# Kernel tuning notes

Measured on AMD Instinct MI355X. Metric: run time of the kernel, lower is better.

## Reference

```python
import jax, jax.numpy as jnp
import numpy as np

N_NODES = 50000
N_EDGES = 800000  # includes N_NODES self-loops so every node has in-degree >= 1
D_IN = 64
D_OUT = 64


def setup_inputs() -> dict:
    key = jax.random.key(0)
    k_feat, k_src, k_dst, k_wt, k_wp = jax.random.split(key, 5)
    feat = jax.random.normal(k_feat, (N_NODES, D_IN), dtype=jnp.float32)
    n_rand = N_EDGES - N_NODES
    loops = jnp.arange(N_NODES, dtype=jnp.int64)
    src = jnp.concatenate([loops, jax.random.randint(k_src, (n_rand,), 0, N_NODES, dtype=jnp.int64)])
    dst = jnp.concatenate([loops, jax.random.randint(k_dst, (n_rand,), 0, N_NODES, dtype=jnp.int64)])
    scale = 1.0 / np.sqrt(D_IN)
    W_theta = jax.random.normal(k_wt, (D_IN, D_OUT), dtype=jnp.float32) * scale
    b_theta = jnp.zeros((D_OUT,), dtype=jnp.float32)
    W_phi = jax.random.normal(k_wp, (D_IN, D_OUT), dtype=jnp.float32) * scale
    b_phi = jnp.zeros((D_OUT,), dtype=jnp.float32)
    return {"feat": feat, "src": src, "dst": dst,
            "W_theta": W_theta, "b_theta": b_theta,
            "W_phi": W_phi, "b_phi": b_phi}


def reference(feat, src, dst, W_theta, b_theta, W_phi, b_phi):
    # Per-edge message: theta(x_dst - x_src)  [fn.v_sub_u then Dense theta]
    diff = feat[dst] - feat[src]                       # [E, D_in]
    theta_e = diff @ W_theta + b_theta                 # [E, D_out]
    # Per-destination-node term: phi(x_dst)  [Dense phi]
    phi = feat @ W_phi + b_phi                         # [N, D_out]
    e = theta_e + phi[dst]                             # [E, D_out]  (fn.e_add_v)
    # Scatter-max aggregation by destination node (fn.max)
    out = jax.ops.segment_max(e, dst, num_segments=feat.shape[0])  # [N, D_out]
    return out
```

## Files before the change

### kernel.cpp

```cpp
#include <hip/hip_runtime.h>
#include <hip/hip_bf16.h>

#define N_NODES 50000
#define N_EDGES 800000
#define D 64
#define NB 391
#define BCAP 4096
#define CHUNK_E 2048
#define NSC 391
#define NSTRIP 3125
#define GEMM_BLKS 196
#define NWAVES 784
#define SPW 4

typedef __attribute__((ext_vector_type(8))) short short8v;
typedef __attribute__((ext_vector_type(4))) float float4v;

__device__ __forceinline__ float b2f(unsigned short h) {
    return __uint_as_float(((unsigned)h) << 16);
}
__device__ __forceinline__ unsigned short f2b(float f) {
    __hip_bfloat16 t = __float2bfloat16(f);
    return *reinterpret_cast<unsigned short*>(&t);
}
__device__ __forceinline__ short f2bs(float f) { return (short)f2b(f); }
__device__ __forceinline__ unsigned f2ord(float f) {
    unsigned u = __float_as_uint(f);
    return (u & 0x80000000u) ? ~u : (u | 0x80000000u);
}
__device__ __forceinline__ float ord2f(unsigned o) {
    return __uint_as_float((o & 0x80000000u) ? (o ^ 0x80000000u) : ~o);
}

__global__ __launch_bounds__(256)
void setup(const void* __restrict__ featv, const void* __restrict__ srcv,
           const void* __restrict__ Wtv, const void* __restrict__ btv,
           const void* __restrict__ Wpv, const void* __restrict__ bpv,
           unsigned* __restrict__ flags, unsigned* __restrict__ c_cur,
           unsigned short* __restrict__ WTfrag, unsigned short* __restrict__ WPfrag,
           float* __restrict__ bias_sum) {
    __shared__ unsigned sf[2];
    const int t = threadIdx.x;
    if (t < 64) {
        const unsigned short* p = (const unsigned short*)featv;
        float x = b2f(p[2 * t]);
        float a = fabsf(x);
        bool insane = !(a <= 64.f) || (x != 0.f && a < 9.3132e-10f);
        unsigned long long m = __ballot(insane);
        if (t == 0) sf[0] = (__popcll(m) >= 8) ? 1u : 0u;
    } else if (t < 128) {
        const int* s32 = (const int*)srcv;
        int v = s32[2 * (t - 64) + 1];
        unsigned long long m = __ballot(v == 0);
        if (t == 64) sf[1] = (__popcll(m) >= 32) ? 1u : 0u;
    }
    __syncthreads();
    const unsigned fp32mode = sf[0];
    if (t < 2) flags[t] = sf[t];
    for (int i = t; i < NB; i += 256) c_cur[i] = 0;
#pragma unroll
    for (int i = 0; i < 16; ++i) {
        int e = i * 256 + t;
        int k = e >> 6, n = e & 63;
        float vt, vp;
        if (fp32mode) {
            vt = ((const float*)Wtv)[e];
            vp = ((const float*)Wpv)[e];
        } else {
            vt = b2f(((const unsigned short*)Wtv)[e]);
            vp = b2f(((const unsigned short*)Wpv)[e]);
        }
        WTfrag[n * 64 + k] = f2b(vt);
        WPfrag[n * 64 + k] = f2b(vp);
    }
    if (t < 64) {
        if (fp32mode)
            bias_sum[t] = ((const float*)btv)[t] + ((const float*)bpv)[t];
        else
            bias_sum[t] = b2f(((const unsigned short*)btv)[t])
                        + b2f(((const unsigned short*)bpv)[t]);
    }
}

__device__ __forceinline__ void loadA_bf16(const short* F, int w, int m, int q,
                                           short8v& A0, short8v& A1) {
    const short* fr = F + (w * 16 + m) * D + q * 8;
    A0 = *(const short8v*)fr;
    A1 = *(const short8v*)(fr + 32);
}
__device__ __forceinline__ void loadA_raw(const float* F, int w, int m, int q,
                                          float4 r[8]) {
    const float* fr = F + (w * 16 + m) * D + q * 8;
    r[0] = *(const float4*)(fr);      r[1] = *(const float4*)(fr + 4);
    r[2] = *(const float4*)(fr + 32); r[3] = *(const float4*)(fr + 36);
}
__device__ __forceinline__ void cvtA(const float4 r[8], short8v& A0, short8v& A1) {
    A0 = (short8v){f2bs(r[0].x), f2bs(r[0].y), f2bs(r[0].z), f2bs(r[0].w),
                   f2bs(r[1].x), f2bs(r[1].y), f2bs(r[1].z), f2bs(r[1].w)};
    A1 = (short8v){f2bs(r[2].x), f2bs(r[2].y), f2bs(r[2].z), f2bs(r[2].w),
                   f2bs(r[3].x), f2bs(r[3].y), f2bs(r[3].z), f2bs(r[3].w)};
}

__global__ __launch_bounds__(256)
void gemm_scatter(const void* __restrict__ featv,
                  const unsigned short* __restrict__ WTfrag,
                  const unsigned short* __restrict__ WPfrag,
                  const float* __restrict__ bias_sum,
                  const void* __restrict__ srcv, const void* __restrict__ dstv,
                  const unsigned* __restrict__ flags,
                  unsigned* __restrict__ c_cur, unsigned* __restrict__ packed,
                  unsigned short* __restrict__ T16, void* __restrict__ outv) {
    const unsigned fp32mode = flags[0];
    if (blockIdx.x < GEMM_BLKS) {
        const int lane = threadIdx.x & 63;
        const int wid  = threadIdx.x >> 6;
        const int wave = blockIdx.x * 4 + wid;
        const int m = lane & 15, q = lane >> 4;

        const short8v* BT = (const short8v*)WTfrag;
        const short8v* BP = (const short8v*)WPfrag;
        short8v Bt0[4], Bt1[4], Bp0[4], Bp1[4];
        float bsv[4];
#pragma unroll
        for (int c = 0; c < 4; ++c) {
            const int col = 16 * c + m;
            Bt0[c] = BT[col * 8 + q];
            Bt1[c] = BT[col * 8 + 4 + q];
            Bp0[c] = BP[col * 8 + q];
            Bp1[c] = BP[col * 8 + 4 + q];
            bsv[c] = bias_sum[col];
        }

        float* Cf  = (float*)outv;
        unsigned short* Ch = (unsigned short*)outv;
        const float* Ff = (const float*)featv;
        const short* Fh = (const short*)featv;

        short8v A0, A1;
        float4 raw[8];
        int w = wave;
        if (fp32mode) { loadA_raw(Ff, min(w, NSTRIP - 1), m, q, raw); cvtA(raw, A0, A1); }
        else          loadA_bf16(Fh, min(w, NSTRIP - 1), m, q, A0, A1);

#pragma unroll
        for (int s = 0; s < SPW; ++s) {
            const int wn = wave + (s + 1) * NWAVES;
            if (s + 1 < SPW) {
                if (fp32mode) loadA_raw(Ff, min(wn, NSTRIP - 1), m, q, raw);
                else          loadA_bf16(Fh, min(wn, NSTRIP - 1), m, q, A0, A1);
            }
            if (w < NSTRIP) {
                short8v Acur0, Acur1;
                if (s + 1 < SPW && !fp32mode) {
                    loadA_bf16(Fh, w, m, q, Acur0, Acur1);
                } else if (!fp32mode) {
                    Acur0 = A0; Acur1 = A1;
                } else {
                    Acur0 = A0; Acur1 = A1;
                }
#pragma unroll
                for (int c = 0; c < 4; ++c) {
                    float4v accT = (float4v){0.f, 0.f, 0.f, 0.f};
                    float4v accP = (float4v){bsv[c], bsv[c], bsv[c], bsv[c]};
                    accT = __builtin_amdgcn_mfma_f32_16x16x32_bf16(Acur0, Bt0[c], accT, 0, 0, 0);
                    accT = __builtin_amdgcn_mfma_f32_16x16x32_bf16(Acur1, Bt1[c], accT, 0, 0, 0);
                    accP = __builtin_amdgcn_mfma_f32_16x16x32_bf16(Acur0, Bp0[c], accP, 0, 0, 0);
                    accP = __builtin_amdgcn_mfma_f32_16x16x32_bf16(Acur1, Bp1[c], accP, 0, 0, 0);
                    const int col = 16 * c + m;
#pragma unroll
                    for (int r = 0; r < 4; ++r) {
                        const int row = w * 16 + q * 4 + r;
                        T16[row * D + col] = f2b(accT[r]);
                        if (fp32mode) Cf[row * D + col] = accT[r] + accP[r];
                        else          Ch[row * D + col] = f2b(accT[r] + accP[r]);
                    }
                }
            }
            w = wn;
            if (fp32mode && s + 1 < SPW) cvtA(raw, A0, A1);
        }
    } else {
        __shared__ unsigned h[NB];
        const int t = threadIdx.x;
        for (int i = t; i < NB; i += 256) h[i] = 0;
        __syncthreads();
        const unsigned idx64 = flags[1];
        const int base = (blockIdx.x - GEMM_BLKS) * CHUNK_E;
        unsigned pk[CHUNK_E / 256];
#pragma unroll
        for (int j = 0; j < CHUNK_E / 256; ++j) {
            int e = base + j * 256 + t;
            unsigned p = 0xFFFFFFFFu;
            if (e < N_EDGES) {
                int s, d;
                if (idx64) {
                    s = (int)((const long long*)srcv)[e];
                    d = (int)((const long long*)dstv)[e];
                } else {
                    s = ((const int*)srcv)[e];
                    d = ((const int*)dstv)[e];
                }
                s = min(max(s, 0), N_NODES - 1);
                d = min(max(d, 0), N_NODES - 1);
                if (s != d) {
                    p = ((unsigned)d << 16) | (unsigned)s;
                    atomicAdd(&h[d >> 7], 1u);
                }
            }
            pk[j] = p;
        }
        __syncthreads();
        for (int i = t; i < NB; i += 256) h[i] = atomicAdd(&c_cur[i], h[i]);
        __syncthreads();
#pragma unroll
        for (int j = 0; j < CHUNK_E / 256; ++j) {
            unsigned p = pk[j];
            if (p != 0xFFFFFFFFu) {
                unsigned bkt = p >> 23;
                unsigned pos = atomicAdd(&h[bkt], 1u);
                if (pos < BCAP)
                    packed[bkt * BCAP + pos] = p;
            }
        }
    }
}

__global__ __launch_bounds__(512)
void bucket_min(const unsigned* __restrict__ c_cur, const unsigned* __restrict__ packed,
                const unsigned short* __restrict__ T16, const unsigned* __restrict__ flags,
                void* __restrict__ outv) {
    __shared__ unsigned mn[128 * 64];
    const unsigned fp32mode = flags[0];
    const int t = threadIdx.x;
    const int b = blockIdx.x;
    const int node0 = b << 7;
    for (int sl = t; sl < 128 * 16; sl += 512) {
        const int row = sl >> 4;
        const int f4 = (sl & 15) << 2;
        unsigned* mp = &mn[row * 64 + f4];
        if (node0 + row < N_NODES) {
            uint2 v = *(const uint2*)(T16 + (node0 + row) * D + f4);
            mp[0] = f2ord(b2f((unsigned short)v.x));
            mp[1] = f2ord(b2f((unsigned short)(v.x >> 16)));
            mp[2] = f2ord(b2f((unsigned short)v.y));
            mp[3] = f2ord(b2f((unsigned short)(v.y >> 16)));
        } else {
            mp[0] = mp[1] = mp[2] = mp[3] = 0xFFFFFFFFu;
        }
    }
    __syncthreads();
    const int cnt = min((int)c_cur[b], BCAP);
    const unsigned* pb = packed + b * BCAP;
    const int lane = t & 63, wv = t >> 6;
    const int g = lane >> 4, fb = (lane & 15) << 2;
    int i = wv * 4 + g;
    for (; i + 96 < cnt; i += 128) {
        unsigned p0 = pb[i],      p1 = pb[i + 32];
        unsigned p2 = pb[i + 64], p3 = pb[i + 96];
        uint2 v0 = *(const uint2*)(T16 + (int)(p0 & 0xFFFFu) * D + fb);
        uint2 v1 = *(const uint2*)(T16 + (int)(p1 & 0xFFFFu) * D + fb);
        uint2 v2 = *(const uint2*)(T16 + (int)(p2 & 0xFFFFu) * D + fb);
        uint2 v3 = *(const uint2*)(T16 + (int)(p3 & 0xFFFFu) * D + fb);
        unsigned* m0p = &mn[(int)((p0 >> 16) & 127u) * 64 + fb];
        unsigned* m1p = &mn[(int)((p1 >> 16) & 127u) * 64 + fb];
        unsigned* m2p = &mn[(int)((p2 >> 16) & 127u) * 64 + fb];
        unsigned* m3p = &mn[(int)((p3 >> 16) & 127u) * 64 + fb];
        atomicMin(m0p + 0, f2ord(b2f((unsigned short)v0.x)));
        atomicMin(m0p + 1, f2ord(b2f((unsigned short)(v0.x >> 16))));
        atomicMin(m0p + 2, f2ord(b2f((unsigned short)v0.y)));
        atomicMin(m0p + 3, f2ord(b2f((unsigned short)(v0.y >> 16))));
        atomicMin(m1p + 0, f2ord(b2f((unsigned short)v1.x)));
        atomicMin(m1p + 1, f2ord(b2f((unsigned short)(v1.x >> 16))));
        atomicMin(m1p + 2, f2ord(b2f((unsigned short)v1.y)));
        atomicMin(m1p + 3, f2ord(b2f((unsigned short)(v1.y >> 16))));
        atomicMin(m2p + 0, f2ord(b2f((unsigned short)v2.x)));
        atomicMin(m2p + 1, f2ord(b2f((unsigned short)(v2.x >> 16))));
        atomicMin(m2p + 2, f2ord(b2f((unsigned short)v2.y)));
        atomicMin(m2p + 3, f2ord(b2f((unsigned short)(v2.y >> 16))));
        atomicMin(m3p + 0, f2ord(b2f((unsigned short)v3.x)));
        atomicMin(m3p + 1, f2ord(b2f((unsigned short)(v3.x >> 16))));
        atomicMin(m3p + 2, f2ord(b2f((unsigned short)v3.y)));
        atomicMin(m3p + 3, f2ord(b2f((unsigned short)(v3.y >> 16))));
    }
    for (; i < cnt; i += 32) {
        unsigned p0 = pb[i];
        uint2 v0 = *(const uint2*)(T16 + (int)(p0 & 0xFFFFu) * D + fb);
        unsigned* m0p = &mn[(int)((p0 >> 16) & 127u) * 64 + fb];
        atomicMin(m0p + 0, f2ord(b2f((unsigned short)v0.x)));
        atomicMin(m0p + 1, f2ord(b2f((unsigned short)(v0.x >> 16))));
        atomicMin(m0p + 2, f2ord(b2f((unsigned short)v0.y)));
        atomicMin(m0p + 3, f2ord(b2f((unsigned short)(v0.y >> 16))));
    }
    __syncthreads();
    for (int sl = t; sl < 128 * 16; sl += 512) {
        const int row = sl >> 4;
        const int node = node0 + row;
        if (node >= N_NODES) break;
        const int f4 = (sl & 15) << 2;
        const unsigned* mp = &mn[row * 64 + f4];
        float m0 = ord2f(mp[0]), m1 = ord2f(mp[1]);
        float m2 = ord2f(mp[2]), m3 = ord2f(mp[3]);
        if (fp32mode) {
            float4* C = (float4*)((float*)outv + node * D + f4);
            float4 c = *C;
            *C = make_float4(c.x - m0, c.y - m1, c.z - m2, c.w - m3);
        } else {
            unsigned short* C = (unsigned short*)outv + node * D + f4;
            uint2 c = *(uint2*)C;
            unsigned lo = (unsigned)f2b(b2f((unsigned short)c.x) - m0)
                        | ((unsigned)f2b(b2f((unsigned short)(c.x >> 16)) - m1) << 16);
            unsigned hi = (unsigned)f2b(b2f((unsigned short)c.y) - m2)
                        | ((unsigned)f2b(b2f((unsigned short)(c.y >> 16)) - m3) << 16);
            *(uint2*)C = make_uint2(lo, hi);
        }
    }
}

extern "C" void kernel_launch(void* const* d_in, const int* in_sizes, int n_in,
                              void* d_out, int out_size, void* d_ws, size_t ws_size,
                              hipStream_t stream) {
    char* p = (char*)d_ws;
    unsigned*       flags    = (unsigned*)p;
    unsigned*       c_cur    = (unsigned*)(p + 256);
    unsigned*       packed   = (unsigned*)(p + 4352);
    unsigned short* T16      = (unsigned short*)(p + 4352 + 6406144);
    unsigned short* WTfrag   = (unsigned short*)(p + 4352 + 6406144 + 6400000);
    unsigned short* WPfrag   = (unsigned short*)(p + 4352 + 6406144 + 6400000 + 8192);
    float*          bias_sum = (float*)(p + 4352 + 6406144 + 6400000 + 16384);

    setup<<<1, 256, 0, stream>>>(d_in[0], d_in[1], d_in[3], d_in[4], d_in[5], d_in[6],
                                 flags, c_cur, WTfrag, WPfrag, bias_sum);
    gemm_scatter<<<GEMM_BLKS + NSC, 256, 0, stream>>>(d_in[0], WTfrag, WPfrag, bias_sum,
                                                      d_in[1], d_in[2], flags,
                                                      c_cur, packed, T16, d_out);
    bucket_min<<<NB, 512, 0, stream>>>(c_cur, packed, T16, flags, d_out);
}
```

Before: 128.9 us.

## Use finer 32-node destination buckets with padded LDS and 16-byte gathers

Destination buckets shrink from 128 nodes to 32 nodes, giving 1563 buckets of capacity 1024 and 256-thread bucket_min blocks, so many more blocks run concurrently. Each lane now gathers 8 bf16 features per edge with a 16-byte load. The shared min table uses a 65-word row stride to cut LDS bank conflicts during atomicMin. The scatter phase also skips the global atomicAdd for empty buckets. The trade-offs are more global bucket counters and a smaller per-bucket capacity that could overflow on skewed degree distributions.

```diff
diff --git a/kernel.cpp b/kernel.cpp
--- a/kernel.cpp
+++ b/kernel.cpp
@@ -4,14 +4,15 @@
 #define N_NODES 50000
 #define N_EDGES 800000
 #define D 64
-#define NB 391
-#define BCAP 4096
+#define NB 1563
+#define BCAP 1024
 #define CHUNK_E 2048
 #define NSC 391
 #define NSTRIP 3125
 #define GEMM_BLKS 196
 #define NWAVES 784
 #define SPW 4
+#define MSTR 65
 
 typedef __attribute__((ext_vector_type(8))) short short8v;
 typedef __attribute__((ext_vector_type(4))) float float4v;
@@ -204,19 +205,22 @@
                 d = min(max(d, 0), N_NODES - 1);
                 if (s != d) {
                     p = ((unsigned)d << 16) | (unsigned)s;
-                    atomicAdd(&h[d >> 7], 1u);
+                    atomicAdd(&h[d >> 5], 1u);
                 }
             }
             pk[j] = p;
         }
         __syncthreads();
-        for (int i = t; i < NB; i += 256) h[i] = atomicAdd(&c_cur[i], h[i]);
+        for (int i = t; i < NB; i += 256) {
+            unsigned c = h[i];
+            h[i] = c ? atomicAdd(&c_cur[i], c) : 0u;
+        }
         __syncthreads();
 #pragma unroll
         for (int j = 0; j < CHUNK_E / 256; ++j) {
             unsigned p = pk[j];
             if (p != 0xFFFFFFFFu) {
-                unsigned bkt = p >> 23;
+                unsigned bkt = p >> 21;
                 unsigned pos = atomicAdd(&h[bkt], 1u);
                 if (pos < BCAP)
                     packed[bkt * BCAP + pos] = p;
@@ -225,19 +229,19 @@
     }
 }
 
-__global__ __launch_bounds__(512)
+__global__ __launch_bounds__(256, 8)
 void bucket_min(const unsigned* __restrict__ c_cur, const unsigned* __restrict__ packed,
                 const unsigned short* __restrict__ T16, const unsigned* __restrict__ flags,
                 void* __restrict__ outv) {
-    __shared__ unsigned mn[128 * 64];
+    __shared__ unsigned mn[32 * MSTR];
     const unsigned fp32mode = flags[0];
     const int t = threadIdx.x;
     const int b = blockIdx.x;
-    const int node0 = b << 7;
-    for (int sl = t; sl < 128 * 16; sl += 512) {
+    const int node0 = b << 5;
+    for (int sl = t; sl < 32 * 16; sl += 256) {
         const int row = sl >> 4;
         const int f4 = (sl & 15) << 2;
-        unsigned* mp = &mn[row * 64 + f4];
+        unsigned* mp = &mn[row * MSTR + f4];
         if (node0 + row < N_NODES) {
             uint2 v = *(const uint2*)(T16 + (node0 + row) * D + f4);
             mp[0] = f2ord(b2f((unsigned short)v.x));
@@ -252,52 +256,53 @@
     const int cnt = min((int)c_cur[b], BCAP);
     const unsigned* pb = packed + b * BCAP;
     const int lane = t & 63, wv = t >> 6;
-    const int g = lane >> 4, fb = (lane & 15) << 2;
-    int i = wv * 4 + g;
-    for (; i + 96 < cnt; i += 128) {
-        unsigned p0 = pb[i],      p1 = pb[i + 32];
-        unsigned p2 = pb[i + 64], p3 = pb[i + 96];
-        uint2 v0 = *(const uint2*)(T16 + (int)(p0 & 0xFFFFu) * D + fb);
-        uint2 v1 = *(const uint2*)(T16 + (int)(p1 & 0xFFFFu) * D + fb);
-        uint2 v2 = *(const uint2*)(T16 + (int)(p2 & 0xFFFFu) * D + fb);
-        uint2 v3 = *(const uint2*)(T16 + (int)(p3 & 0xFFFFu) * D + fb);
-        unsigned* m0p = &mn[(int)((p0 >> 16) & 127u) * 64 + fb];
-        unsigned* m1p = &mn[(int)((p1 >> 16) & 127u) * 64 + fb];
-        unsigned* m2p = &mn[(int)((p2 >> 16) & 127u) * 64 + fb];
-        unsigned* m3p = &mn[(int)((p3 >> 16) & 127u) * 64 + fb];
+    const int g = lane >> 3;
+    const int fh = (lane & 7) << 3;
+    const int fu = (lane & 7) << 3;
+    int i = wv * 8 + g;
+    for (; i + 32 < cnt; i += 64) {
+        unsigned p0 = pb[i], p1 = pb[i + 32];
+        uint4 v0 = *(const uint4*)(T16 + (int)(p0 & 0xFFFFu) * D + fh);
+        uint4 v1 = *(const uint4*)(T16 + (int)(p1 & 0xFFFFu) * D + fh);
+        unsigned* m0p = &mn[(int)((p0 >> 16) & 31u) * MSTR + fu];
+        unsigned* m1p = &mn[(int)((p1 >> 16) & 31u) * MSTR + fu];
         atomicMin(m0p + 0, f2ord(b2f((unsigned short)v0.x)));
         atomicMin(m0p + 1, f2ord(b2f((unsigned short)(v0.x >> 16))));
         atomicMin(m0p + 2, f2ord(b2f((unsigned short)v0.y)));
         atomicMin(m0p + 3, f2ord(b2f((unsigned short)(v0.y >> 16))));
+        atomicMin(m0p + 4, f2ord(b2f((unsigned short)v0.z)));
+        atomicMin(m0p + 5, f2ord(b2f((unsigned short)(v0.z >> 16))));
+        atomicMin(m0p + 6, f2ord(b2f((unsigned short)v0.w)));
+        atomicMin(m0p + 7, f2ord(b2f((unsigned short)(v0.w >> 16))));
         atomicMin(m1p + 0, f2ord(b2f((unsigned short)v1.x)));
         atomicMin(m1p + 1, f2ord(b2f((unsigned short)(v1.x >> 16))));
         atomicMin(m1p + 2, f2ord(b2f((unsigned short)v1.y)));
         atomicMin(m1p + 3, f2ord(b2f((unsigned short)(v1.y >> 16))));
-        atomicMin(m2p + 0, f2ord(b2f((unsigned short)v2.x)));
-        atomicMin(m2p + 1, f2ord(b2f((unsigned short)(v2.x >> 16))));
-        atomicMin(m2p + 2, f2ord(b2f((unsigned short)v2.y)));
-        atomicMin(m2p + 3, f2ord(b2f((unsigned short)(v2.y >> 16))));
-        atomicMin(m3p + 0, f2ord(b2f((unsigned short)v3.x)));
-        atomicMin(m3p + 1, f2ord(b2f((unsigned short)(v3.x >> 16))));
-        atomicMin(m3p + 2, f2ord(b2f((unsigned short)v3.y)));
-        atomicMin(m3p + 3, f2ord(b2f((unsigned short)(v3.y >> 16))));
+        atomicMin(m1p + 4, f2ord(b2f((unsigned short)v1.z)));
+        atomicMin(m1p + 5, f2ord(b2f((unsigned short)(v1.z >> 16))));
+        atomicMin(m1p + 6, f2ord(b2f((unsigned short)v1.w)));
+        atomicMin(m1p + 7, f2ord(b2f((unsigned short)(v1.w >> 16))));
     }
     for (; i < cnt; i += 32) {
         unsigned p0 = pb[i];
-        uint2 v0 = *(const uint2*)(T16 + (int)(p0 & 0xFFFFu) * D + fb);
-        unsigned* m0p = &mn[(int)((p0 >> 16) & 127u) * 64 + fb];
+        uint4 v0 = *(const uint4*)(T16 + (int)(p0 & 0xFFFFu) * D + fh);
+        unsigned* m0p = &mn[(int)((p0 >> 16) & 31u) * MSTR + fu];
         atomicMin(m0p + 0, f2ord(b2f((unsigned short)v0.x)));
         atomicMin(m0p + 1, f2ord(b2f((unsigned short)(v0.x >> 16))));
         atomicMin(m0p + 2, f2ord(b2f((unsigned short)v0.y)));
         atomicMin(m0p + 3, f2ord(b2f((unsigned short)(v0.y >> 16))));
+        atomicMin(m0p + 4, f2ord(b2f((unsigned short)v0.z)));
+        atomicMin(m0p + 5, f2ord(b2f((unsigned short)(v0.z >> 16))));
+        atomicMin(m0p + 6, f2ord(b2f((unsigned short)v0.w)));
+        atomicMin(m0p + 7, f2ord(b2f((unsigned short)(v0.w >> 16))));
     }
     __syncthreads();
-    for (int sl = t; sl < 128 * 16; sl += 512) {
+    for (int sl = t; sl < 32 * 16; sl += 256) {
         const int row = sl >> 4;
         const int node = node0 + row;
-        if (node >= N_NODES) break;
+        if (node >= N_NODES) continue;
         const int f4 = (sl & 15) << 2;
-        const unsigned* mp = &mn[row * 64 + f4];
+        const unsigned* mp = &mn[row * MSTR + f4];
         float m0 = ord2f(mp[0]), m1 = ord2f(mp[1]);
         float m2 = ord2f(mp[2]), m3 = ord2f(mp[3]);
         if (fp32mode) {
@@ -322,16 +327,16 @@
     char* p = (char*)d_ws;
     unsigned*       flags    = (unsigned*)p;
     unsigned*       c_cur    = (unsigned*)(p + 256);
-    unsigned*       packed   = (unsigned*)(p + 4352);
-    unsigned short* T16      = (unsigned short*)(p + 4352 + 6406144);
-    unsigned short* WTfrag   = (unsigned short*)(p + 4352 + 6406144 + 6400000);
-    unsigned short* WPfrag   = (unsigned short*)(p + 4352 + 6406144 + 6400000 + 8192);
-    float*          bias_sum = (float*)(p + 4352 + 6406144 + 6400000 + 16384);
+    unsigned*       packed   = (unsigned*)(p + 8448);
+    unsigned short* T16      = (unsigned short*)(p + 8448 + 6402048);
+    unsigned short* WTfrag   = (unsigned short*)(p + 8448 + 6402048 + 6400000);
+    unsigned short* WPfrag   = (unsigned short*)(p + 8448 + 6402048 + 6400000 + 8192);
+    float*          bias_sum = (float*)(p + 8448 + 6402048 + 6400000 + 16384);
 
     setup<<<1, 256, 0, stream>>>(d_in[0], d_in[1], d_in[3], d_in[4], d_in[5], d_in[6],
                                  flags, c_cur, WTfrag, WPfrag, bias_sum);
     gemm_scatter<<<GEMM_BLKS + NSC, 256, 0, stream>>>(d_in[0], WTfrag, WPfrag, bias_sum,
                                                       d_in[1], d_in[2], flags,
                                                       c_cur, packed, T16, d_out);
-    bucket_min<<<NB, 512, 0, stream>>>(c_cur, packed, T16, flags, d_out);
-}
+    bucket_min<<<NB, 256, 0, stream>>>(c_cur, packed, T16, flags, d_out);
+}
```

New measurement: 123.8 us. 4.0% less time.

## Replace bucketed LDS atomic-min aggregation with per-node CSR lists and register min

Applied to the files above, without the earlier changes.

Edges are now scattered directly into fixed-capacity per-destination lists (16-bit source ids, capacity 64) through global atomic counters, replacing the two-pass per-block bucket histogram. A new node_min kernel gives each node eight threads, each reducing eight features in registers with fminf over the gathered source rows, so the shared-memory ordered-uint atomicMin pass goes away. The GEMM now gives each wave a single strip across more blocks and writes the transposed MFMA output in packed vector stores. The fixed cap of 64 silently drops edges beyond it. Per-node loops also have uneven lengths that can diverge within a wave.

```diff
diff --git a/kernel.cpp b/kernel.cpp
--- a/kernel.cpp
+++ b/kernel.cpp
@@ -4,14 +4,12 @@
 #define N_NODES 50000
 #define N_EDGES 800000
 #define D 64
-#define NB 391
-#define BCAP 4096
+#define CAP 64
 #define CHUNK_E 2048
 #define NSC 391
 #define NSTRIP 3125
-#define GEMM_BLKS 196
-#define NWAVES 784
-#define SPW 4
+#define GEMM_BLKS 782
+#define SETUP_BLKS 64
 
 typedef __attribute__((ext_vector_type(8))) short short8v;
 typedef __attribute__((ext_vector_type(4))) float float4v;
@@ -24,23 +22,19 @@
     return *reinterpret_cast<unsigned short*>(&t);
 }
 __device__ __forceinline__ short f2bs(float f) { return (short)f2b(f); }
-__device__ __forceinline__ unsigned f2ord(float f) {
-    unsigned u = __float_as_uint(f);
-    return (u & 0x80000000u) ? ~u : (u | 0x80000000u);
-}
-__device__ __forceinline__ float ord2f(unsigned o) {
-    return __uint_as_float((o & 0x80000000u) ? (o ^ 0x80000000u) : ~o);
-}
 
 __global__ __launch_bounds__(256)
 void setup(const void* __restrict__ featv, const void* __restrict__ srcv,
            const void* __restrict__ Wtv, const void* __restrict__ btv,
            const void* __restrict__ Wpv, const void* __restrict__ bpv,
-           unsigned* __restrict__ flags, unsigned* __restrict__ c_cur,
+           unsigned* __restrict__ flags, unsigned* __restrict__ cnt,
            unsigned short* __restrict__ WTfrag, unsigned short* __restrict__ WPfrag,
            float* __restrict__ bias_sum) {
+    const int t = threadIdx.x;
+    for (int i = blockIdx.x * 256 + t; i < N_NODES; i += SETUP_BLKS * 256) cnt[i] = 0;
+    if (blockIdx.x != 0) return;
+
     __shared__ unsigned sf[2];
-    const int t = threadIdx.x;
     if (t < 64) {
         const unsigned short* p = (const unsigned short*)featv;
         float x = b2f(p[2 * t]);
@@ -57,7 +51,6 @@
     __syncthreads();
     const unsigned fp32mode = sf[0];
     if (t < 2) flags[t] = sf[t];
-    for (int i = t; i < NB; i += 256) c_cur[i] = 0;
 #pragma unroll
     for (int i = 0; i < 16; ++i) {
         int e = i * 256 + t;
@@ -108,19 +101,20 @@
                   const float* __restrict__ bias_sum,
                   const void* __restrict__ srcv, const void* __restrict__ dstv,
                   const unsigned* __restrict__ flags,
-                  unsigned* __restrict__ c_cur, unsigned* __restrict__ packed,
+                  unsigned* __restrict__ cnt, unsigned short* __restrict__ packed16,
                   unsigned short* __restrict__ T16, void* __restrict__ outv) {
     const unsigned fp32mode = flags[0];
     if (blockIdx.x < GEMM_BLKS) {
         const int lane = threadIdx.x & 63;
         const int wid  = threadIdx.x >> 6;
-        const int wave = blockIdx.x * 4 + wid;
+        const int w = blockIdx.x * 4 + wid;
+        if (w >= NSTRIP) return;
         const int m = lane & 15, q = lane >> 4;
 
         const short8v* BT = (const short8v*)WTfrag;
         const short8v* BP = (const short8v*)WPfrag;
         short8v Bt0[4], Bt1[4], Bp0[4], Bp1[4];
-        float bsv[4];
+        float4 bs4[4];
 #pragma unroll
         for (int c = 0; c < 4; ++c) {
             const int col = 16 * c + m;
@@ -128,69 +122,52 @@
             Bt1[c] = BT[col * 8 + 4 + q];
             Bp0[c] = BP[col * 8 + q];
             Bp1[c] = BP[col * 8 + 4 + q];
-            bsv[c] = bias_sum[col];
-        }
-
-        float* Cf  = (float*)outv;
-        unsigned short* Ch = (unsigned short*)outv;
-        const float* Ff = (const float*)featv;
-        const short* Fh = (const short*)featv;
+            bs4[c] = *(const float4*)(bias_sum + 16 * c + 4 * q);
+        }
 
         short8v A0, A1;
-        float4 raw[8];
-        int w = wave;
-        if (fp32mode) { loadA_raw(Ff, min(w, NSTRIP - 1), m, q, raw); cvtA(raw, A0, A1); }
-        else          loadA_bf16(Fh, min(w, NSTRIP - 1), m, q, A0, A1);
-
-#pragma unroll
-        for (int s = 0; s < SPW; ++s) {
-            const int wn = wave + (s + 1) * NWAVES;
-            if (s + 1 < SPW) {
-                if (fp32mode) loadA_raw(Ff, min(wn, NSTRIP - 1), m, q, raw);
-                else          loadA_bf16(Fh, min(wn, NSTRIP - 1), m, q, A0, A1);
+        if (fp32mode) {
+            float4 raw[8];
+            loadA_raw((const float*)featv, w, m, q, raw);
+            cvtA(raw, A0, A1);
+        } else {
+            loadA_bf16((const short*)featv, w, m, q, A0, A1);
+        }
+
+        const int node = w * 16 + m;
+        unsigned short* Trow = T16 + node * D;
+        float* Cf = (float*)outv + node * D;
+        unsigned short* Ch = (unsigned short*)outv + node * D;
+#pragma unroll
+        for (int c = 0; c < 4; ++c) {
+            float4v accT = (float4v){0.f, 0.f, 0.f, 0.f};
+            float4v accP = (float4v){bs4[c].x, bs4[c].y, bs4[c].z, bs4[c].w};
+            accT = __builtin_amdgcn_mfma_f32_16x16x32_bf16(Bt0[c], A0, accT, 0, 0, 0);
+            accT = __builtin_amdgcn_mfma_f32_16x16x32_bf16(Bt1[c], A1, accT, 0, 0, 0);
+            accP = __builtin_amdgcn_mfma_f32_16x16x32_bf16(Bp0[c], A0, accP, 0, 0, 0);
+            accP = __builtin_amdgcn_mfma_f32_16x16x32_bf16(Bp1[c], A1, accP, 0, 0, 0);
+            const int foff = 16 * c + 4 * q;
+            unsigned t0 = (unsigned)f2b(accT[0]) | ((unsigned)f2b(accT[1]) << 16);
+            unsigned t1 = (unsigned)f2b(accT[2]) | ((unsigned)f2b(accT[3]) << 16);
+            *(uint2*)(Trow + foff) = make_uint2(t0, t1);
+            if (fp32mode) {
+                *(float4*)(Cf + foff) = make_float4(accT[0] + accP[0], accT[1] + accP[1],
+                                                    accT[2] + accP[2], accT[3] + accP[3]);
+            } else {
+                unsigned c0 = (unsigned)f2b(accT[0] + accP[0])
+                            | ((unsigned)f2b(accT[1] + accP[1]) << 16);
+                unsigned c1 = (unsigned)f2b(accT[2] + accP[2])
+                            | ((unsigned)f2b(accT[3] + accP[3]) << 16);
+                *(uint2*)(Ch + foff) = make_uint2(c0, c1);
             }
-            if (w < NSTRIP) {
-                short8v Acur0, Acur1;
-                if (s + 1 < SPW && !fp32mode) {
-                    loadA_bf16(Fh, w, m, q, Acur0, Acur1);
-                } else if (!fp32mode) {
-                    Acur0 = A0; Acur1 = A1;
-                } else {
-                    Acur0 = A0; Acur1 = A1;
-                }
-#pragma unroll
-                for (int c = 0; c < 4; ++c) {
-                    float4v accT = (float4v){0.f, 0.f, 0.f, 0.f};
-                    float4v accP = (float4v){bsv[c], bsv[c], bsv[c], bsv[c]};
-                    accT = __builtin_amdgcn_mfma_f32_16x16x32_bf16(Acur0, Bt0[c], accT, 0, 0, 0);
-                    accT = __builtin_amdgcn_mfma_f32_16x16x32_bf16(Acur1, Bt1[c], accT, 0, 0, 0);
-                    accP = __builtin_amdgcn_mfma_f32_16x16x32_bf16(Acur0, Bp0[c], accP, 0, 0, 0);
-                    accP = __builtin_amdgcn_mfma_f32_16x16x32_bf16(Acur1, Bp1[c], accP, 0, 0, 0);
-                    const int col = 16 * c + m;
-#pragma unroll
-                    for (int r = 0; r < 4; ++r) {
-                        const int row = w * 16 + q * 4 + r;
-                        T16[row * D + col] = f2b(accT[r]);
-                        if (fp32mode) Cf[row * D + col] = accT[r] + accP[r];
-                        else          Ch[row * D + col] = f2b(accT[r] + accP[r]);
-                    }
-                }
-            }
-            w = wn;
-            if (fp32mode && s + 1 < SPW) cvtA(raw, A0, A1);
         }
     } else {
-        __shared__ unsigned h[NB];
-        const int t = threadIdx.x;
-        for (int i = t; i < NB; i += 256) h[i] = 0;
-        __syncthreads();
         const unsigned idx64 = flags[1];
         const int base = (blockIdx.x - GEMM_BLKS) * CHUNK_E;
-        unsigned pk[CHUNK_E / 256];
+        const int t = threadIdx.x;
 #pragma unroll
         for (int j = 0; j < CHUNK_E / 256; ++j) {
             int e = base + j * 256 + t;
-            unsigned p = 0xFFFFFFFFu;
             if (e < N_EDGES) {
                 int s, d;
                 if (idx64) {
@@ -203,116 +180,77 @@
                 s = min(max(s, 0), N_NODES - 1);
                 d = min(max(d, 0), N_NODES - 1);
                 if (s != d) {
-                    p = ((unsigned)d << 16) | (unsigned)s;
-                    atomicAdd(&h[d >> 7], 1u);
+                    unsigned pos = atomicAdd(&cnt[d], 1u);
+                    if (pos < CAP)
+                        packed16[(unsigned)d * CAP + pos] = (unsigned short)s;
                 }
             }
-            pk[j] = p;
-        }
-        __syncthreads();
-        for (int i = t; i < NB; i += 256) h[i] = atomicAdd(&c_cur[i], h[i]);
-        __syncthreads();
-#pragma unroll
-        for (int j = 0; j < CHUNK_E / 256; ++j) {
-            unsigned p = pk[j];
-            if (p != 0xFFFFFFFFu) {
-                unsigned bkt = p >> 23;
-                unsigned pos = atomicAdd(&h[bkt], 1u);
-                if (pos < BCAP)
-                    packed[bkt * BCAP + pos] = p;
-            }
-        }
-    }
-}
-
-__global__ __launch_bounds__(512)
-void bucket_min(const unsigned* __restrict__ c_cur, const unsigned* __restrict__ packed,
-                const unsigned short* __restrict__ T16, const unsigned* __restrict__ flags,
-                void* __restrict__ outv) {
-    __shared__ unsigned mn[128 * 64];
+        }
+    }
+}
+
+#define MIN8(vv)                                                     \
+    do {                                                             \
+        mn[0] = fminf(mn[0], b2f((unsigned short)(vv).x));           \
+        mn[1] = fminf(mn[1], b2f((unsigned short)((vv).x >> 16)));   \
+        mn[2] = fminf(mn[2], b2f((unsigned short)(vv).y));           \
+        mn[3] = fminf(mn[3], b2f((unsigned short)((vv).y >> 16)));   \
+        mn[4] = fminf(mn[4], b2f((unsigned short)(vv).z));           \
+        mn[5] = fminf(mn[5], b2f((unsigned short)((vv).z >> 16)));   \
+        mn[6] = fminf(mn[6], b2f((unsigned short)((vv).w)));         \
+        mn[7] = fminf(mn[7], b2f((unsigned short)((vv).w >> 16)));   \
+    } while (0)
+
+__global__ __launch_bounds__(256, 4)
+void node_min(const unsigned* __restrict__ cnt, const unsigned short* __restrict__ packed16,
+              const unsigned short* __restrict__ T16, const unsigned* __restrict__ flags,
+              void* __restrict__ outv) {
     const unsigned fp32mode = flags[0];
     const int t = threadIdx.x;
-    const int b = blockIdx.x;
-    const int node0 = b << 7;
-    for (int sl = t; sl < 128 * 16; sl += 512) {
-        const int row = sl >> 4;
-        const int f4 = (sl & 15) << 2;
-        unsigned* mp = &mn[row * 64 + f4];
-        if (node0 + row < N_NODES) {
-            uint2 v = *(const uint2*)(T16 + (node0 + row) * D + f4);
-            mp[0] = f2ord(b2f((unsigned short)v.x));
-            mp[1] = f2ord(b2f((unsigned short)(v.x >> 16)));
-            mp[2] = f2ord(b2f((unsigned short)v.y));
-            mp[3] = f2ord(b2f((unsigned short)(v.y >> 16)));
-        } else {
-            mp[0] = mp[1] = mp[2] = mp[3] = 0xFFFFFFFFu;
-        }
-    }
-    __syncthreads();
-    const int cnt = min((int)c_cur[b], BCAP);
-    const unsigned* pb = packed + b * BCAP;
-    const int lane = t & 63, wv = t >> 6;
-    const int g = lane >> 4, fb = (lane & 15) << 2;
-    int i = wv * 4 + g;
-    for (; i + 96 < cnt; i += 128) {
-        unsigned p0 = pb[i],      p1 = pb[i + 32];
-        unsigned p2 = pb[i + 64], p3 = pb[i + 96];
-        uint2 v0 = *(const uint2*)(T16 + (int)(p0 & 0xFFFFu) * D + fb);
-        uint2 v1 = *(const uint2*)(T16 + (int)(p1 & 0xFFFFu) * D + fb);
-        uint2 v2 = *(const uint2*)(T16 + (int)(p2 & 0xFFFFu) * D + fb);
-        uint2 v3 = *(const uint2*)(T16 + (int)(p3 & 0xFFFFu) * D + fb);
-        unsigned* m0p = &mn[(int)((p0 >> 16) & 127u) * 64 + fb];
-        unsigned* m1p = &mn[(int)((p1 >> 16) & 127u) * 64 + fb];
-        unsigned* m2p = &mn[(int)((p2 >> 16) & 127u) * 64 + fb];
-        unsigned* m3p = &mn[(int)((p3 >> 16) & 127u) * 64 + fb];
-        atomicMin(m0p + 0, f2ord(b2f((unsigned short)v0.x)));
-        atomicMin(m0p + 1, f2ord(b2f((unsigned short)(v0.x >> 16))));
-        atomicMin(m0p + 2, f2ord(b2f((unsigned short)v0.y)));
-        atomicMin(m0p + 3, f2ord(b2f((unsigned short)(v0.y >> 16))));
-        atomicMin(m1p + 0, f2ord(b2f((unsigned short)v1.x)));
-        atomicMin(m1p + 1, f2ord(b2f((unsigned short)(v1.x >> 16))));
-        atomicMin(m1p + 2, f2ord(b2f((unsigned short)v1.y)));
-        atomicMin(m1p + 3, f2ord(b2f((unsigned short)(v1.y >> 16))));
-        atomicMin(m2p + 0, f2ord(b2f((unsigned short)v2.x)));
-        atomicMin(m2p + 1, f2ord(b2f((unsigned short)(v2.x >> 16))));
-        atomicMin(m2p + 2, f2ord(b2f((unsigned short)v2.y)));
-        atomicMin(m2p + 3, f2ord(b2f((unsigned short)(v2.y >> 16))));
-        atomicMin(m3p + 0, f2ord(b2f((unsigned short)v3.x)));
-        atomicMin(m3p + 1, f2ord(b2f((unsigned short)(v3.x >> 16))));
-        atomicMin(m3p + 2, f2ord(b2f((unsigned short)v3.y)));
-        atomicMin(m3p + 3, f2ord(b2f((unsigned short)(v3.y >> 16))));
-    }
-    for (; i < cnt; i += 32) {
-        unsigned p0 = pb[i];
-        uint2 v0 = *(const uint2*)(T16 + (int)(p0 & 0xFFFFu) * D + fb);
-        unsigned* m0p = &mn[(int)((p0 >> 16) & 127u) * 64 + fb];
-        atomicMin(m0p + 0, f2ord(b2f((unsigned short)v0.x)));
-        atomicMin(m0p + 1, f2ord(b2f((unsigned short)(v0.x >> 16))));
-        atomicMin(m0p + 2, f2ord(b2f((unsigned short)v0.y)));
-        atomicMin(m0p + 3, f2ord(b2f((unsigned short)(v0.y >> 16))));
-    }
-    __syncthreads();
-    for (int sl = t; sl < 128 * 16; sl += 512) {
-        const int row = sl >> 4;
-        const int node = node0 + row;
-        if (node >= N_NODES) break;
-        const int f4 = (sl & 15) << 2;
-        const unsigned* mp = &mn[row * 64 + f4];
-        float m0 = ord2f(mp[0]), m1 = ord2f(mp[1]);
-        float m2 = ord2f(mp[2]), m3 = ord2f(mp[3]);
-        if (fp32mode) {
-            float4* C = (float4*)((float*)outv + node * D + f4);
-            float4 c = *C;
-            *C = make_float4(c.x - m0, c.y - m1, c.z - m2, c.w - m3);
-        } else {
-            unsigned short* C = (unsigned short*)outv + node * D + f4;
-            uint2 c = *(uint2*)C;
-            unsigned lo = (unsigned)f2b(b2f((unsigned short)c.x) - m0)
-                        | ((unsigned)f2b(b2f((unsigned short)(c.x >> 16)) - m1) << 16);
-            unsigned hi = (unsigned)f2b(b2f((unsigned short)c.y) - m2)
-                        | ((unsigned)f2b(b2f((unsigned short)(c.y >> 16)) - m3) << 16);
-            *(uint2*)C = make_uint2(lo, hi);
-        }
+    const int g = t >> 3, sub = t & 7;
+    const int node = blockIdx.x * 32 + g;
+    if (node >= N_NODES) return;
+    const int fo = sub * 8;
+    float mn[8];
+    {
+        uint4 v = *(const uint4*)(T16 + node * D + fo);
+        mn[0] = b2f((unsigned short)v.x); mn[1] = b2f((unsigned short)(v.x >> 16));
+        mn[2] = b2f((unsigned short)v.y); mn[3] = b2f((unsigned short)(v.y >> 16));
+        mn[4] = b2f((unsigned short)v.z); mn[5] = b2f((unsigned short)(v.z >> 16));
+        mn[6] = b2f((unsigned short)v.w); mn[7] = b2f((unsigned short)(v.w >> 16));
+    }
+    const int c = min((int)cnt[node], CAP);
+    const unsigned short* pl = packed16 + (unsigned)node * CAP;
+    if (c > 0) {
+        uint4 v = *(const uint4*)(T16 + (int)pl[0] * D + fo);
+        for (int i = 1; i < c; ++i) {
+            uint4 vn = *(const uint4*)(T16 + (int)pl[i] * D + fo);
+            MIN8(v);
+            v = vn;
+        }
+        MIN8(v);
+    }
+    if (fp32mode) {
+        float* Crow = (float*)outv + node * D + fo;
+        float4 a = *(const float4*)Crow;
+        float4 b = *(const float4*)(Crow + 4);
+        a.x -= mn[0]; a.y -= mn[1]; a.z -= mn[2]; a.w -= mn[3];
+        b.x -= mn[4]; b.y -= mn[5]; b.z -= mn[6]; b.w -= mn[7];
+        *(float4*)Crow = a;
+        *(float4*)(Crow + 4) = b;
+    } else {
+        unsigned short* Crow = (unsigned short*)outv + node * D + fo;
+        uint4 cb = *(const uint4*)Crow;
+        uint4 o;
+        o.x = (unsigned)f2b(b2f((unsigned short)cb.x) - mn[0])
+            | ((unsigned)f2b(b2f((unsigned short)(cb.x >> 16)) - mn[1]) << 16);
+        o.y = (unsigned)f2b(b2f((unsigned short)cb.y) - mn[2])
+            | ((unsigned)f2b(b2f((unsigned short)(cb.y >> 16)) - mn[3]) << 16);
+        o.z = (unsigned)f2b(b2f((unsigned short)cb.z) - mn[4])
+            | ((unsigned)f2b(b2f((unsigned short)(cb.z >> 16)) - mn[5]) << 16);
+        o.w = (unsigned)f2b(b2f((unsigned short)cb.w) - mn[6])
+            | ((unsigned)f2b(b2f((unsigned short)(cb.w >> 16)) - mn[7]) << 16);
+        *(uint4*)Crow = o;
     }
 }
 
@@ -321,17 +259,17 @@
                               hipStream_t stream) {
     char* p = (char*)d_ws;
     unsigned*       flags    = (unsigned*)p;
-    unsigned*       c_cur    = (unsigned*)(p + 256);
-    unsigned*       packed   = (unsigned*)(p + 4352);
-    unsigned short* T16      = (unsigned short*)(p + 4352 + 6406144);
-    unsigned short* WTfrag   = (unsigned short*)(p + 4352 + 6406144 + 6400000);
-    unsigned short* WPfrag   = (unsigned short*)(p + 4352 + 6406144 + 6400000 + 8192);
-    float*          bias_sum = (float*)(p + 4352 + 6406144 + 6400000 + 16384);
-
-    setup<<<1, 256, 0, stream>>>(d_in[0], d_in[1], d_in[3], d_in[4], d_in[5], d_in[6],
-                                 flags, c_cur, WTfrag, WPfrag, bias_sum);
+    unsigned*       cnt      = (unsigned*)(p + 256);
+    unsigned short* packed16 = (unsigned short*)(p + 200960);
+    unsigned short* T16      = (unsigned short*)(p + 200960 + 6400000);
+    unsigned short* WTfrag   = (unsigned short*)(p + 200960 + 12800000);
+    unsigned short* WPfrag   = (unsigned short*)(p + 200960 + 12800000 + 8192);
+    float*          bias_sum = (float*)(p + 200960 + 12800000 + 16384);
+
+    setup<<<SETUP_BLKS, 256, 0, stream>>>(d_in[0], d_in[1], d_in[3], d_in[4], d_in[5], d_in[6],
+                                          flags, cnt, WTfrag, WPfrag, bias_sum);
     gemm_scatter<<<GEMM_BLKS + NSC, 256, 0, stream>>>(d_in[0], WTfrag, WPfrag, bias_sum,
                                                       d_in[1], d_in[2], flags,
-                                                      c_cur, packed, T16, d_out);
-    bucket_min<<<NB, 512, 0, stream>>>(c_cur, packed, T16, flags, d_out);
-}
+                                                      cnt, packed16, T16, d_out);
+    node_min<<<(N_NODES + 31) / 32, 256, 0, stream>>>(cnt, packed16, T16, flags, d_out);
+}
```

Result: slower. 173.7 us (+34.8%).
